# Performance work log

Measured on AMD Instinct MI355X. Metric: run time of the kernel, lower is better.

Reference implementation:

```python
import jax, jax.numpy as jnp
import numpy as np

N = 100_000      # nodes
E = 1_600_000    # edges
D_IN = 128       # input_dim
H = 128          # hidden_dim
L = 3            # num_layers
G = 128          # graphs in batch
EPS = 1e-5       # BatchNorm1d eps


def setup_inputs() -> dict:
    key = jax.random.key(0)
    ks = jax.random.split(key, 8)
    inp = {
        "x": jax.random.normal(ks[0], (N, D_IN), dtype=jnp.float32),
        "edge_index": jax.random.randint(ks[1], (2, E), 0, N),
        "batch": jnp.sort(jax.random.randint(ks[2], (N,), 0, G)),
    }
    for i in range(L):
        din = D_IN if i == 0 else H
        kw = jax.random.fold_in(key, 100 + i)
        inp[f"W{i}"] = jax.random.normal(kw, (din, H), dtype=jnp.float32) / np.sqrt(din).astype(np.float32)
        inp[f"b{i}"] = jnp.zeros((H,), jnp.float32)
        inp[f"g{i}"] = jnp.ones((H,), jnp.float32)
        inp[f"beta{i}"] = jnp.zeros((H,), jnp.float32)
    return inp


def _gcn_conv(x, W, b, src, dst, dinv):
    # GCNConv (normalize=True, add_self_loops=True):
    # out = D^{-1/2} (A + I) D^{-1/2} X W + b, deg computed on dst with self-loops
    h = x @ W                                   # [N,H]
    coef = (dinv[src] * dinv[dst])[:, None]     # per-edge norm
    agg = jax.ops.segment_sum(h[src] * coef, dst, num_segments=N)
    agg = agg + h * (dinv * dinv)[:, None]      # self-loop term deg^{-1}
    return agg + b


def _batchnorm(z, g, beta):
    mu = jnp.mean(z, axis=0)
    var = jnp.mean(jnp.square(z - mu), axis=0)  # biased var (training-mode BN)
    return (z - mu) * jax.lax.rsqrt(var + EPS) * g + beta


def reference(x, edge_index, batch,
              W0, b0, g0, beta0,
              W1, b1, g1, beta1,
              W2, b2, g2, beta2):
    src, dst = edge_index[0], edge_index[1]
    # degree of A + I on target index
    deg = jax.ops.segment_sum(jnp.ones((E,), x.dtype), dst, num_segments=N) + 1.0
    dinv = jax.lax.rsqrt(deg)
    params = [(W0, b0, g0, beta0), (W1, b1, g1, beta1), (W2, b2, g2, beta2)]
    zs = []
    h = x
    for (W, b, g, beta) in params:
        h = _gcn_conv(h, W, b, src, dst, dinv)
        h = jax.nn.relu(h)
        h = _batchnorm(h, g, beta)
        zs.append(h)
    pooled = [jax.ops.segment_sum(z, batch, num_segments=G) for z in zs]  # sum pool
    h_cat = jnp.concatenate(zs, axis=1)        # [N, L*H]
    g_cat = jnp.concatenate(pooled, axis=1)    # [G, L*H]
    return h_cat, g_cat
```

## Files before the change

kernel.cpp:

```cpp
#include <hip/hip_runtime.h>

#define NN 100000
#define NE 1600000
#define NG 128
#define BN_EPS 1e-5f
#define NBKT 64
#define AGG_BLOCKS 2048
#define AGG_WAVES (AGG_BLOCKS * 4)
#define NBUCK 98
#define BIN_BLOCKS 256
#define BIN_CHUNK 6250

typedef short s16x8 __attribute__((ext_vector_type(8)));
typedef float f32x4 __attribute__((ext_vector_type(4)));

static __device__ __forceinline__ unsigned short f2bf(float f) {
    unsigned u = __float_as_uint(f);
    u += 0x7fffu + ((u >> 16) & 1u);
    return (unsigned short)(u >> 16);
}
static __device__ __forceinline__ unsigned packbf(float a, float b) {
    return (unsigned)f2bf(a) | ((unsigned)f2bf(b) << 16);
}
static __device__ __forceinline__ float bf_lo(unsigned u) { return __uint_as_float(u << 16); }
static __device__ __forceinline__ float bf_hi(unsigned u) { return __uint_as_float(u & 0xffff0000u); }
static __device__ __forceinline__ float bf2f(ushort u) { return __uint_as_float((unsigned)u << 16); }

__global__ __launch_bounds__(256) void k_bhist(const int* __restrict__ dst, int* __restrict__ gbh) {
    __shared__ int lh[128];
    int t = threadIdx.x;
    if (t < 128) lh[t] = 0;
    __syncthreads();
    for (int e = blockIdx.x * 256 + t; e < NE; e += gridDim.x * 256)
        atomicAdd(&lh[dst[e] >> 10], 1);
    __syncthreads();
    if (t < 128 && lh[t]) atomicAdd(&gbh[t], lh[t]);
}

__global__ __launch_bounds__(128) void k_bscan(const int* __restrict__ gbh, int* __restrict__ gbase,
                                               int* __restrict__ gcur, int* __restrict__ row_start) {
    __shared__ int s[128];
    int t = threadIdx.x;
    int v = gbh[t];
    s[t] = v;
    __syncthreads();
    for (int o = 1; o < 128; o <<= 1) {
        int a = (t >= o) ? s[t - o] : 0;
        __syncthreads();
        s[t] += a;
        __syncthreads();
    }
    int ex = s[t] - v;
    gbase[t] = ex;
    gcur[t] = ex;
    if (t == 127) { gbase[128] = s[127]; row_start[NN] = NE; }
}

__global__ __launch_bounds__(256) void k_bin(const int* __restrict__ src, const int* __restrict__ dst,
                                             int* __restrict__ gcur, int* __restrict__ tmp) {
    __shared__ int lh[128], lb[128], lc[128];
    int t = threadIdx.x;
    if (t < 128) lh[t] = 0;
    __syncthreads();
    int e0 = blockIdx.x * BIN_CHUNK, e1 = e0 + BIN_CHUNK;
    for (int e = e0 + t; e < e1; e += 256) atomicAdd(&lh[dst[e] >> 10], 1);
    __syncthreads();
    if (t < 128) {
        int c = lh[t];
        lb[t] = c ? atomicAdd(&gcur[t], c) : 0;
        lc[t] = 0;
    }
    __syncthreads();
    for (int e = e0 + t; e < e1; e += 256) {
        int d = dst[e];
        int b = d >> 10;
        int off = atomicAdd(&lc[b], 1);
        tmp[lb[b] + off] = (src[e] << 10) | (d & 1023);
    }
}

__global__ __launch_bounds__(256) void k_csr(const int* __restrict__ tmp, const int* __restrict__ gbase,
                                             int* __restrict__ esrc, int* __restrict__ row_start,
                                             float* __restrict__ dinv) {
    __shared__ int h[1024], hs[1024], part[256];
    int b = blockIdx.x, t = threadIdx.x;
    int base = gbase[b], end = gbase[b + 1];
#pragma unroll
    for (int k = 0; k < 4; ++k) h[t * 4 + k] = 0;
    __syncthreads();
    for (int i = base + t; i < end; i += 256) atomicAdd(&h[tmp[i] & 1023], 1);
    __syncthreads();
    int l0 = h[t * 4], l1 = h[t * 4 + 1], l2 = h[t * 4 + 2], l3 = h[t * 4 + 3];
    int ssum = l0 + l1 + l2 + l3;
    part[t] = ssum;
    __syncthreads();
    for (int o = 1; o < 256; o <<= 1) {
        int a = (t >= o) ? part[t - o] : 0;
        __syncthreads();
        part[t] += a;
        __syncthreads();
    }
    int ex = part[t] - ssum;
    hs[t * 4]     = ex;
    hs[t * 4 + 1] = ex + l0;
    hs[t * 4 + 2] = ex + l0 + l1;
    hs[t * 4 + 3] = ex + l0 + l1 + l2;
    int n0 = b * 1024 + t * 4;
#pragma unroll
    for (int k = 0; k < 4; ++k) {
        int n = n0 + k;
        if (n < NN) {
            row_start[n] = base + hs[t * 4 + k];
            dinv[n] = rsqrtf((float)h[t * 4 + k] + 1.0f);
        }
    }
    __syncthreads();
    for (int i = base + t; i < end; i += 256) {
        int rec = tmp[i];
        int pos = atomicAdd(&hs[rec & 1023], 1);
        esrc[base + pos] = rec >> 10;
    }
}

__global__ __launch_bounds__(256) void k_cast(const float* __restrict__ x, uint4* __restrict__ xb) {
    int i = blockIdx.x * 256 + threadIdx.x;
    if (i >= NN * 16) return;
    float4 a = *(const float4*)(x + (size_t)i * 8);
    float4 b = *(const float4*)(x + (size_t)i * 8 + 4);
    uint4 o;
    o.x = packbf(a.x, a.y);
    o.y = packbf(a.z, a.w);
    o.z = packbf(b.x, b.y);
    o.w = packbf(b.z, b.w);
    xb[i] = o;
}

__global__ __launch_bounds__(64) void k_wfrag(const float* __restrict__ W, ushort* __restrict__ Wf) {
    int unit = blockIdx.x;
    int lane = threadIdx.x;
    int ks = unit >> 3, nb = unit & 7;
    int n = nb * 16 + (lane & 15);
    int k0 = ks * 32 + (lane >> 4) * 8;
    ushort o[8];
#pragma unroll
    for (int j = 0; j < 8; ++j) o[j] = f2bf(W[(size_t)(k0 + j) * 128 + n]);
    ushort* p = Wf + ((size_t)unit * 64 + lane) * 8;
#pragma unroll
    for (int j = 0; j < 8; ++j) p[j] = o[j];
}

__global__ __launch_bounds__(64) void k_wscale(const ushort* __restrict__ Wfb, const float* __restrict__ svec,
                                               ushort* __restrict__ Wff) {
    int unit = blockIdx.x;
    int lane = threadIdx.x;
    int k0 = (unit >> 3) * 32 + (lane >> 4) * 8;
    const ushort* p = Wfb + ((size_t)unit * 64 + lane) * 8;
    ushort* o = Wff + ((size_t)unit * 64 + lane) * 8;
#pragma unroll
    for (int j = 0; j < 8; ++j) o[j] = f2bf(bf2f(p[j]) * svec[k0 + j]);
}

__global__ __launch_bounds__(128) void k_finalize(const float* __restrict__ S, const float* __restrict__ Q,
                                                  const float* __restrict__ gam, const float* __restrict__ bet,
                                                  float* __restrict__ svec, float* __restrict__ tvec,
                                                  const float* __restrict__ Wnext, float* __restrict__ tW) {
    __shared__ float ts[128];
    int c = threadIdx.x;
    float s = 0.f, q = 0.f;
    for (int k = 0; k < NBKT; ++k) {
        s += S[k * 128 + c];
        q += Q[k * 128 + c];
    }
    float mean = s / (float)NN;
    float var = q / (float)NN - mean * mean;
    float rstd = rsqrtf(fmaxf(var, 0.f) + BN_EPS);
    float sc = gam[c] * rstd;
    float sh = bet[c] - mean * sc;
    svec[c] = sc;
    tvec[c] = sh;
    ts[c] = sh;
    __syncthreads();
    if (Wnext) {
        float acc = 0.f;
        for (int k = 0; k < 128; ++k) acc += ts[k] * Wnext[(size_t)k * 128 + c];
        tW[c] = acc;
    }
}

__global__ __launch_bounds__(256) void k_gemm(const ushort* __restrict__ Xb, const ushort* __restrict__ Wf,
                                              const float* __restrict__ tW, const float* __restrict__ dinv,
                                              ushort* __restrict__ hm) {
    int tid = threadIdx.x;
    int wid = tid >> 6, lane = tid & 63;
    int r0 = blockIdx.x * 64 + wid * 16;
    int m = lane & 15, g = lane >> 4;
    int xrow = r0 + m;
    int xr = (xrow < NN) ? xrow : (NN - 1);
    const ushort* Xrow = Xb + (size_t)xr * 128 + g * 8;
    f32x4 acc[8];
#pragma unroll
    for (int nb = 0; nb < 8; ++nb) acc[nb] = (f32x4){0.f, 0.f, 0.f, 0.f};
#pragma unroll
    for (int ks = 0; ks < 4; ++ks) {
        s16x8 af = *(const s16x8*)(Xrow + ks * 32);
#pragma unroll
        for (int nb = 0; nb < 8; ++nb) {
            s16x8 wf = *(const s16x8*)(Wf + ((size_t)(ks * 8 + nb) * 64 + lane) * 8);
            acc[nb] = __builtin_amdgcn_mfma_f32_16x16x32_bf16(wf, af, acc[nb], 0, 0, 0);
        }
    }
    if (xrow < NN) {
        float ds = dinv[xr];
        ushort* orow = hm + (size_t)xrow * 128 + g * 4;
        if (tW) {
#pragma unroll
            for (int nb = 0; nb < 8; ++nb) {
                float4 tw = *(const float4*)(tW + nb * 16 + g * 4);
                ushort4 o;
                o.x = f2bf(ds * (acc[nb][0] + tw.x));
                o.y = f2bf(ds * (acc[nb][1] + tw.y));
                o.z = f2bf(ds * (acc[nb][2] + tw.z));
                o.w = f2bf(ds * (acc[nb][3] + tw.w));
                *(ushort4*)(orow + nb * 16) = o;
            }
        } else {
#pragma unroll
            for (int nb = 0; nb < 8; ++nb) {
                ushort4 o;
                o.x = f2bf(ds * acc[nb][0]);
                o.y = f2bf(ds * acc[nb][1]);
                o.z = f2bf(ds * acc[nb][2]);
                o.w = f2bf(ds * acc[nb][3]);
                *(ushort4*)(orow + nb * 16) = o;
            }
        }
    }
}

__global__ __launch_bounds__(256) void k_agg(const uint* __restrict__ hm32, const int* __restrict__ esrc,
                                             const int* __restrict__ rs, const float* __restrict__ dinv,
                                             const float* __restrict__ bias, uint* __restrict__ act,
                                             float* __restrict__ bnsum, float* __restrict__ bnsq) {
    __shared__ float ls[128], lq[128];
    int tid = threadIdx.x;
    if (tid < 128) { ls[tid] = 0.f; lq[tid] = 0.f; }
    __syncthreads();
    int lane = tid & 63;
    int wgid = blockIdx.x * 4 + (tid >> 6);
    float2 b2 = *(const float2*)(bias + lane * 2);
    float s0 = 0.f, s1 = 0.f, q0 = 0.f, q1 = 0.f;

    for (int n = wgid; n < NN; n += AGG_WAVES) {
        uint self = hm32[(size_t)n * 64 + lane];
        float a0 = bf_lo(self);
        float a1 = bf_hi(self);

        int i  = __builtin_amdgcn_readfirstlane(rs[n]);
        int i1 = __builtin_amdgcn_readfirstlane(rs[n + 1]);

        int idxv = 0;
        if (i < i1) idxv = esrc[i + min(min(lane, 15), i1 - i - 1)];

        while (i < i1) {
            int cnt = i1 - i;
            cnt = (cnt > 16) ? 16 : cnt;
            int cur = idxv;
            int inext = i + cnt;
            if (inext < i1)
                idxv = esrc[inext + min(min(lane, 15), i1 - inext - 1)];
            uint g[16];
#pragma unroll
            for (int u = 0; u < 16; ++u) {
                int sidx = __builtin_amdgcn_readlane(cur, u);
                sidx = (u < cnt) ? sidx : NN;
                g[u] = hm32[(size_t)sidx * 64 + lane];
            }
#pragma unroll
            for (int u = 0; u < 16; ++u) {
                a0 += bf_lo(g[u]);
                a1 += bf_hi(g[u]);
            }
            i = inext;
        }
        float di = dinv[n];
        float z0 = fmaxf(fmaf(di, a0, b2.x), 0.f);
        float z1 = fmaxf(fmaf(di, a1, b2.y), 0.f);
        act[(size_t)n * 64 + lane] = packbf(z0, z1);
        s0 += z0; s1 += z1;
        q0 += z0 * z0; q1 += z1 * z1;
    }
    atomicAdd(&ls[lane * 2],     s0);
    atomicAdd(&ls[lane * 2 + 1], s1);
    atomicAdd(&lq[lane * 2],     q0);
    atomicAdd(&lq[lane * 2 + 1], q1);
    __syncthreads();
    if (tid < 128) {
        int bkt = blockIdx.x & (NBKT - 1);
        atomicAdd(&bnsum[bkt * 128 + tid], ls[tid]);
        atomicAdd(&bnsq[bkt * 128 + tid],  lq[tid]);
    }
}

__global__ __launch_bounds__(128) void k_norm(const ushort* __restrict__ act, const float* __restrict__ svec,
                                              const float* __restrict__ tvec, const int* __restrict__ batch,
                                              float* __restrict__ out, float* __restrict__ gout, int lofs) {
    int c = threadIdx.x;
    int n0 = blockIdx.x * 64;
    if (n0 >= NN) return;
    int n1 = n0 + 64; if (n1 > NN) n1 = NN;
    float scale = svec[c];
    float shift = tvec[c];
    int cur = batch[n0];
    float acc = 0.f;
    for (int n = n0; n < n1; ++n) {
        float z = bf2f(act[(size_t)n * 128 + c]) * scale + shift;
        out[(size_t)n * 384 + lofs + c] = z;
        int bn = batch[n];
        if (bn != cur) {
            atomicAdd(&gout[(size_t)cur * 384 + lofs + c], acc);
            acc = 0.f;
            cur = bn;
        }
        acc += z;
    }
    atomicAdd(&gout[(size_t)cur * 384 + lofs + c], acc);
}

extern "C" void kernel_launch(void* const* d_in, const int* in_sizes, int n_in,
                              void* d_out, int out_size, void* d_ws, size_t ws_size,
                              hipStream_t stream) {
    const float* x = (const float*)d_in[0];
    const int* ei = (const int*)d_in[1];
    const int* src = ei;
    const int* dst = ei + NE;
    const int* batch = (const int*)d_in[2];
    const float *W[3], *b[3], *g[3], *beta[3];
    for (int l = 0; l < 3; ++l) {
        W[l]    = (const float*)d_in[3 + 4 * l];
        b[l]    = (const float*)d_in[4 + 4 * l];
        g[l]    = (const float*)d_in[5 + 4 * l];
        beta[l] = (const float*)d_in[6 + 4 * l];
    }
    float* out = (float*)d_out;
    float* gout = out + (size_t)NN * 384;

    char* ws = (char*)d_ws;
    size_t off = 0;
    auto alloc = [&](size_t bytes) -> char* {
        off = (off + 255) & ~(size_t)255;
        char* p = ws + off;
        off += bytes;
        return p;
    };
    ushort* xb       = (ushort*)alloc((size_t)NN * 256);
    ushort* act      = (ushort*)alloc((size_t)NN * 256);
    ushort* hm       = (ushort*)alloc((size_t)(NN + 1) * 256);
    int*    esrc     = (int*)alloc((size_t)NE * 4);
    int*    tmp      = (int*)alloc((size_t)NE * 4);
    int*    row_start= (int*)alloc((size_t)(NN + 1) * 4);
    float*  dinv     = (float*)alloc((size_t)NN * 4);
    float*  bnst     = (float*)alloc((size_t)3 * 2 * NBKT * 128 * 4);
    ushort* Wf       = (ushort*)alloc(3 * 16384 * 2);
    ushort* Wff      = (ushort*)alloc(16384 * 2);
    float*  svt      = (float*)alloc(3 * 2 * 128 * 4);
    float*  tW       = (float*)alloc(128 * 4);
    int*    misc     = (int*)alloc(512 * 4);
    int* gbh   = misc;
    int* gbase = misc + 128;
    int* gcur  = misc + 384;
    (void)ws_size;

    hipMemsetAsync(gbh, 0, 128 * 4, stream);
    hipMemsetAsync(hm + (size_t)NN * 128, 0, 256, stream);
    hipMemsetAsync(bnst, 0, (size_t)3 * 2 * NBKT * 128 * 4, stream);
    hipMemsetAsync(gout, 0, (size_t)NG * 384 * 4, stream);

    k_bhist<<<512, 256, 0, stream>>>(dst, gbh);
    k_bscan<<<1, 128, 0, stream>>>(gbh, gbase, gcur, row_start);
    k_bin<<<BIN_BLOCKS, 256, 0, stream>>>(src, dst, gcur, tmp);
    k_csr<<<NBUCK, 256, 0, stream>>>(tmp, gbase, esrc, row_start, dinv);
    k_cast<<<(NN * 16 + 255) / 256, 256, 0, stream>>>(x, (uint4*)xb);
    for (int l = 0; l < 3; ++l) k_wfrag<<<32, 64, 0, stream>>>(W[l], Wf + l * 16384);

    for (int l = 0; l < 3; ++l) {
        float* S = bnst + (size_t)l * 2 * NBKT * 128;
        float* Q = S + NBKT * 128;
        float* sv = svt + l * 256;
        float* tv = sv + 128;
        const ushort* gin = (l == 0) ? xb : act;
        const ushort* wfrag = (l == 0) ? (Wf + 0) : Wff;
        const float* tw_in = (l == 0) ? nullptr : tW;

        k_gemm<<<(NN + 63) / 64, 256, 0, stream>>>(gin, wfrag, tw_in, dinv, hm);
        k_agg<<<AGG_BLOCKS, 256, 0, stream>>>((const uint*)hm, esrc, row_start, dinv, b[l],
                                              (uint*)act, S, Q);
        k_finalize<<<1, 128, 0, stream>>>(S, Q, g[l], beta[l], sv, tv,
                                          (l < 2) ? W[l + 1] : nullptr, tW);
        if (l < 2) k_wscale<<<32, 64, 0, stream>>>(Wf + (l + 1) * 16384, sv, Wff);
        k_norm<<<(NN + 63) / 64, 128, 0, stream>>>(act, sv, tv, batch, out, gout, l * 128);
    }
}
```

Before: 473.1 us.

## Fuse BN output into next-layer GEMM, per-graph pooling, merge finalize and wscale

The normalized output for layers 0 and 1 is now written inside the next layer's GEMM, reusing the bf16 activation tiles it already loads, and only the last layer keeps a standalone normalize kernel. Graph pooling becomes a per-graph reduction over sorted batch ranges (found by binary search) and is written directly instead of using atomics, which also removes the gout memset. BN finalize and weight rescaling are merged into one multi-block launch. The aggregation kernel processes two nodes per wave to raise memory-level parallelism, at the cost of more registers under a launch bound of 8.

```diff
diff --git a/kernel.cpp b/kernel.cpp
--- a/kernel.cpp
+++ b/kernel.cpp
@@ -149,47 +149,76 @@
     for (int j = 0; j < 8; ++j) p[j] = o[j];
 }
 
-__global__ __launch_bounds__(64) void k_wscale(const ushort* __restrict__ Wfb, const float* __restrict__ svec,
-                                               ushort* __restrict__ Wff) {
-    int unit = blockIdx.x;
-    int lane = threadIdx.x;
-    int k0 = (unit >> 3) * 32 + (lane >> 4) * 8;
-    const ushort* p = Wfb + ((size_t)unit * 64 + lane) * 8;
-    ushort* o = Wff + ((size_t)unit * 64 + lane) * 8;
-#pragma unroll
-    for (int j = 0; j < 8; ++j) o[j] = f2bf(bf2f(p[j]) * svec[k0 + j]);
-}
-
-__global__ __launch_bounds__(128) void k_finalize(const float* __restrict__ S, const float* __restrict__ Q,
-                                                  const float* __restrict__ gam, const float* __restrict__ bet,
-                                                  float* __restrict__ svec, float* __restrict__ tvec,
-                                                  const float* __restrict__ Wnext, float* __restrict__ tW) {
-    __shared__ float ts[128];
-    int c = threadIdx.x;
-    float s = 0.f, q = 0.f;
-    for (int k = 0; k < NBKT; ++k) {
-        s += S[k * 128 + c];
-        q += Q[k * 128 + c];
-    }
-    float mean = s / (float)NN;
-    float var = q / (float)NN - mean * mean;
-    float rstd = rsqrtf(fmaxf(var, 0.f) + BN_EPS);
-    float sc = gam[c] * rstd;
-    float sh = bet[c] - mean * sc;
-    svec[c] = sc;
-    tvec[c] = sh;
-    ts[c] = sh;
-    __syncthreads();
-    if (Wnext) {
-        float acc = 0.f;
-        for (int k = 0; k < 128; ++k) acc += ts[k] * Wnext[(size_t)k * 128 + c];
-        tW[c] = acc;
+__global__ __launch_bounds__(128) void k_gbounds(const int* __restrict__ batch, int* __restrict__ gb) {
+    int g = threadIdx.x;
+    int lo = 0, hi = NN;
+    while (lo < hi) {
+        int mid = (lo + hi) >> 1;
+        if (batch[mid] < g) lo = mid + 1; else hi = mid;
+    }
+    gb[g] = lo;
+    if (g == 0) gb[128] = NN;
+}
+
+__global__ __launch_bounds__(128) void k_finwscale(const float* __restrict__ S, const float* __restrict__ Q,
+                                                   const float* __restrict__ gam, const float* __restrict__ bet,
+                                                   float* __restrict__ svec, float* __restrict__ tvec,
+                                                   const float* __restrict__ Wnext, float* __restrict__ tW,
+                                                   const ushort* __restrict__ Wfb, ushort* __restrict__ Wff) {
+    int bid = blockIdx.x;
+    int t = threadIdx.x;
+    if (bid == 0) {
+        __shared__ float ts[128];
+        float s = 0.f, q = 0.f;
+        for (int k = 0; k < NBKT; ++k) {
+            s += S[k * 128 + t];
+            q += Q[k * 128 + t];
+        }
+        float mean = s / (float)NN;
+        float var = q / (float)NN - mean * mean;
+        float rstd = rsqrtf(fmaxf(var, 0.f) + BN_EPS);
+        float sc = gam[t] * rstd;
+        float sh = bet[t] - mean * sc;
+        svec[t] = sc;
+        tvec[t] = sh;
+        ts[t] = sh;
+        __syncthreads();
+        if (Wnext) {
+            float acc = 0.f;
+            for (int k = 0; k < 128; ++k) acc += ts[k] * Wnext[(size_t)k * 128 + t];
+            tW[t] = acc;
+        }
+    } else {
+        __shared__ float sv[32];
+        int unit = bid - 1;
+        int kbase = (unit >> 3) * 32;
+        if (t < 32) {
+            int c = kbase + t;
+            float s = 0.f, q = 0.f;
+            for (int k = 0; k < NBKT; ++k) {
+                s += S[k * 128 + c];
+                q += Q[k * 128 + c];
+            }
+            float mean = s / (float)NN;
+            float var = q / (float)NN - mean * mean;
+            sv[t] = gam[c] * rsqrtf(fmaxf(var, 0.f) + BN_EPS);
+        }
+        __syncthreads();
+        if (t < 64) {
+            int ko = (t >> 4) * 8;
+            const ushort* p = Wfb + ((size_t)unit * 64 + t) * 8;
+            ushort* o = Wff + ((size_t)unit * 64 + t) * 8;
+#pragma unroll
+            for (int j = 0; j < 8; ++j) o[j] = f2bf(bf2f(p[j]) * sv[ko + j]);
+        }
     }
 }
 
 __global__ __launch_bounds__(256) void k_gemm(const ushort* __restrict__ Xb, const ushort* __restrict__ Wf,
                                               const float* __restrict__ tW, const float* __restrict__ dinv,
-                                              ushort* __restrict__ hm) {
+                                              ushort* __restrict__ hm, const float* __restrict__ svec,
+                                              const float* __restrict__ tvec, float* __restrict__ outp,
+                                              int lofs) {
     int tid = threadIdx.x;
     int wid = tid >> 6, lane = tid & 63;
     int r0 = blockIdx.x * 64 + wid * 16;
@@ -197,16 +226,18 @@
     int xrow = r0 + m;
     int xr = (xrow < NN) ? xrow : (NN - 1);
     const ushort* Xrow = Xb + (size_t)xr * 128 + g * 8;
+    s16x8 af[4];
+#pragma unroll
+    for (int ks = 0; ks < 4; ++ks) af[ks] = *(const s16x8*)(Xrow + ks * 32);
     f32x4 acc[8];
 #pragma unroll
     for (int nb = 0; nb < 8; ++nb) acc[nb] = (f32x4){0.f, 0.f, 0.f, 0.f};
 #pragma unroll
     for (int ks = 0; ks < 4; ++ks) {
-        s16x8 af = *(const s16x8*)(Xrow + ks * 32);
 #pragma unroll
         for (int nb = 0; nb < 8; ++nb) {
             s16x8 wf = *(const s16x8*)(Wf + ((size_t)(ks * 8 + nb) * 64 + lane) * 8);
-            acc[nb] = __builtin_amdgcn_mfma_f32_16x16x32_bf16(wf, af, acc[nb], 0, 0, 0);
+            acc[nb] = __builtin_amdgcn_mfma_f32_16x16x32_bf16(wf, af[ks], acc[nb], 0, 0, 0);
         }
     }
     if (xrow < NN) {
@@ -234,13 +265,35 @@
                 *(ushort4*)(orow + nb * 16) = o;
             }
         }
-    }
-}
-
-__global__ __launch_bounds__(256) void k_agg(const uint* __restrict__ hm32, const int* __restrict__ esrc,
-                                             const int* __restrict__ rs, const float* __restrict__ dinv,
-                                             const float* __restrict__ bias, uint* __restrict__ act,
-                                             float* __restrict__ bnsum, float* __restrict__ bnsq) {
+        if (svec) {
+            float* zrow = outp + (size_t)xrow * 384 + lofs;
+#pragma unroll
+            for (int ks = 0; ks < 4; ++ks) {
+                int c0 = ks * 32 + g * 8;
+                float4 s0 = *(const float4*)(svec + c0);
+                float4 s1 = *(const float4*)(svec + c0 + 4);
+                float4 t0 = *(const float4*)(tvec + c0);
+                float4 t1 = *(const float4*)(tvec + c0 + 4);
+                float4 z0, z1;
+                z0.x = bf2f((ushort)af[ks][0]) * s0.x + t0.x;
+                z0.y = bf2f((ushort)af[ks][1]) * s0.y + t0.y;
+                z0.z = bf2f((ushort)af[ks][2]) * s0.z + t0.z;
+                z0.w = bf2f((ushort)af[ks][3]) * s0.w + t0.w;
+                z1.x = bf2f((ushort)af[ks][4]) * s1.x + t1.x;
+                z1.y = bf2f((ushort)af[ks][5]) * s1.y + t1.y;
+                z1.z = bf2f((ushort)af[ks][6]) * s1.z + t1.z;
+                z1.w = bf2f((ushort)af[ks][7]) * s1.w + t1.w;
+                *(float4*)(zrow + c0) = z0;
+                *(float4*)(zrow + c0 + 4) = z1;
+            }
+        }
+    }
+}
+
+__global__ __launch_bounds__(256, 8) void k_agg(const uint* __restrict__ hm32, const int* __restrict__ esrc,
+                                                const int* __restrict__ rs, const float* __restrict__ dinv,
+                                                const float* __restrict__ bias, uint* __restrict__ act,
+                                                float* __restrict__ bnsum, float* __restrict__ bnsq) {
     __shared__ float ls[128], lq[128];
     int tid = threadIdx.x;
     if (tid < 128) { ls[tid] = 0.f; lq[tid] = 0.f; }
@@ -250,44 +303,65 @@
     float2 b2 = *(const float2*)(bias + lane * 2);
     float s0 = 0.f, s1 = 0.f, q0 = 0.f, q1 = 0.f;
 
-    for (int n = wgid; n < NN; n += AGG_WAVES) {
-        uint self = hm32[(size_t)n * 64 + lane];
-        float a0 = bf_lo(self);
-        float a1 = bf_hi(self);
-
-        int i  = __builtin_amdgcn_readfirstlane(rs[n]);
-        int i1 = __builtin_amdgcn_readfirstlane(rs[n + 1]);
-
-        int idxv = 0;
-        if (i < i1) idxv = esrc[i + min(min(lane, 15), i1 - i - 1)];
-
-        while (i < i1) {
-            int cnt = i1 - i;
-            cnt = (cnt > 16) ? 16 : cnt;
-            int cur = idxv;
-            int inext = i + cnt;
-            if (inext < i1)
-                idxv = esrc[inext + min(min(lane, 15), i1 - inext - 1)];
-            uint g[16];
-#pragma unroll
-            for (int u = 0; u < 16; ++u) {
-                int sidx = __builtin_amdgcn_readlane(cur, u);
-                sidx = (u < cnt) ? sidx : NN;
-                g[u] = hm32[(size_t)sidx * 64 + lane];
-            }
-#pragma unroll
-            for (int u = 0; u < 16; ++u) {
-                a0 += bf_lo(g[u]);
-                a1 += bf_hi(g[u]);
-            }
-            i = inext;
-        }
-        float di = dinv[n];
-        float z0 = fmaxf(fmaf(di, a0, b2.x), 0.f);
-        float z1 = fmaxf(fmaf(di, a1, b2.y), 0.f);
-        act[(size_t)n * 64 + lane] = packbf(z0, z1);
-        s0 += z0; s1 += z1;
-        q0 += z0 * z0; q1 += z1 * z1;
+    for (int base = wgid * 2; base < NN; base += AGG_WAVES * 2) {
+        int nA = base, nB = base + 1;
+        uint selfA = hm32[(size_t)nA * 64 + lane];
+        uint selfB = hm32[(size_t)nB * 64 + lane];
+        float aA0 = bf_lo(selfA), aA1 = bf_hi(selfA);
+        float aB0 = bf_lo(selfB), aB1 = bf_hi(selfB);
+
+        int iA  = __builtin_amdgcn_readfirstlane(rs[nA]);
+        int iM  = __builtin_amdgcn_readfirstlane(rs[nA + 1]);
+        int iE  = __builtin_amdgcn_readfirstlane(rs[nB + 1]);
+        int iA1 = iM, iB = iM, iB1 = iE;
+
+        int idxA = 0, idxB = 0;
+        if (iA < iA1) idxA = esrc[iA + min(min(lane, 15), iA1 - iA - 1)];
+        if (iB < iB1) idxB = esrc[iB + min(min(lane, 15), iB1 - iB - 1)];
+
+        while (iA < iA1 || iB < iB1) {
+            int cntA = iA1 - iA; cntA = cntA > 16 ? 16 : (cntA < 0 ? 0 : cntA);
+            int cntB = iB1 - iB; cntB = cntB > 16 ? 16 : (cntB < 0 ? 0 : cntB);
+            int curA = idxA, curB = idxB;
+            int inA = iA + cntA, inB = iB + cntB;
+            if (inA < iA1) idxA = esrc[inA + min(min(lane, 15), iA1 - inA - 1)];
+            if (inB < iB1) idxB = esrc[inB + min(min(lane, 15), iB1 - inB - 1)];
+            uint gA[16], gB[16];
+            if (cntA) {
+#pragma unroll
+                for (int u = 0; u < 16; ++u) {
+                    int sx = __builtin_amdgcn_readlane(curA, u);
+                    sx = (u < cntA) ? sx : NN;
+                    gA[u] = hm32[(size_t)sx * 64 + lane];
+                }
+            }
+            if (cntB) {
+#pragma unroll
+                for (int u = 0; u < 16; ++u) {
+                    int sx = __builtin_amdgcn_readlane(curB, u);
+                    sx = (u < cntB) ? sx : NN;
+                    gB[u] = hm32[(size_t)sx * 64 + lane];
+                }
+            }
+            if (cntA) {
+#pragma unroll
+                for (int u = 0; u < 16; ++u) { aA0 += bf_lo(gA[u]); aA1 += bf_hi(gA[u]); }
+            }
+            if (cntB) {
+#pragma unroll
+                for (int u = 0; u < 16; ++u) { aB0 += bf_lo(gB[u]); aB1 += bf_hi(gB[u]); }
+            }
+            iA = inA; iB = inB;
+        }
+        float dA = dinv[nA], dB = dinv[nB];
+        float zA0 = fmaxf(fmaf(dA, aA0, b2.x), 0.f);
+        float zA1 = fmaxf(fmaf(dA, aA1, b2.y), 0.f);
+        float zB0 = fmaxf(fmaf(dB, aB0, b2.x), 0.f);
+        float zB1 = fmaxf(fmaf(dB, aB1, b2.y), 0.f);
+        act[(size_t)nA * 64 + lane] = packbf(zA0, zA1);
+        act[(size_t)nB * 64 + lane] = packbf(zB0, zB1);
+        s0 += zA0 + zB0; s1 += zA1 + zB1;
+        q0 += zA0 * zA0 + zB0 * zB0; q1 += zA1 * zA1 + zB1 * zB1;
     }
     atomicAdd(&ls[lane * 2],     s0);
     atomicAdd(&ls[lane * 2 + 1], s1);
@@ -301,29 +375,35 @@
     }
 }
 
-__global__ __launch_bounds__(128) void k_norm(const ushort* __restrict__ act, const float* __restrict__ svec,
-                                              const float* __restrict__ tvec, const int* __restrict__ batch,
-                                              float* __restrict__ out, float* __restrict__ gout, int lofs) {
+__global__ __launch_bounds__(256) void k_pool(const ushort* __restrict__ act, const float* __restrict__ svec,
+                                              const float* __restrict__ tvec, const int* __restrict__ gb,
+                                              float* __restrict__ gout, int lofs) {
+    __shared__ float ps[256];
+    int g = blockIdx.x;
+    int t = threadIdx.x;
+    int c = t & 127, half = t >> 7;
+    int gs = gb[g], ge = gb[g + 1];
+    float sum = 0.f;
+    for (int n = gs + half; n < ge; n += 2) sum += bf2f(act[(size_t)n * 128 + c]);
+    ps[t] = sum;
+    __syncthreads();
+    if (t < 128) {
+        float tot = ps[t] + ps[t + 128];
+        float cnt = (float)(ge - gs);
+        gout[(size_t)g * 384 + lofs + t] = svec[t] * tot + tvec[t] * cnt;
+    }
+}
+
+__global__ __launch_bounds__(128) void k_norm2(const ushort* __restrict__ act, const float* __restrict__ svec,
+                                               const float* __restrict__ tvec, float* __restrict__ outp) {
     int c = threadIdx.x;
     int n0 = blockIdx.x * 64;
     if (n0 >= NN) return;
     int n1 = n0 + 64; if (n1 > NN) n1 = NN;
     float scale = svec[c];
     float shift = tvec[c];
-    int cur = batch[n0];
-    float acc = 0.f;
-    for (int n = n0; n < n1; ++n) {
-        float z = bf2f(act[(size_t)n * 128 + c]) * scale + shift;
-        out[(size_t)n * 384 + lofs + c] = z;
-        int bn = batch[n];
-        if (bn != cur) {
-            atomicAdd(&gout[(size_t)cur * 384 + lofs + c], acc);
-            acc = 0.f;
-            cur = bn;
-        }
-        acc += z;
-    }
-    atomicAdd(&gout[(size_t)cur * 384 + lofs + c], acc);
+    for (int n = n0; n < n1; ++n)
+        outp[(size_t)n * 384 + 256 + c] = bf2f(act[(size_t)n * 128 + c]) * scale + shift;
 }
 
 extern "C" void kernel_launch(void* const* d_in, const int* in_sizes, int n_in,
@@ -364,16 +444,16 @@
     ushort* Wff      = (ushort*)alloc(16384 * 2);
     float*  svt      = (float*)alloc(3 * 2 * 128 * 4);
     float*  tW       = (float*)alloc(128 * 4);
-    int*    misc     = (int*)alloc(512 * 4);
+    int*    misc     = (int*)alloc(1024 * 4);
     int* gbh   = misc;
     int* gbase = misc + 128;
     int* gcur  = misc + 384;
+    int* gb    = misc + 512;
     (void)ws_size;
 
     hipMemsetAsync(gbh, 0, 128 * 4, stream);
     hipMemsetAsync(hm + (size_t)NN * 128, 0, 256, stream);
     hipMemsetAsync(bnst, 0, (size_t)3 * 2 * NBKT * 128 * 4, stream);
-    hipMemsetAsync(gout, 0, (size_t)NG * 384 * 4, stream);
 
     k_bhist<<<512, 256, 0, stream>>>(dst, gbh);
     k_bscan<<<1, 128, 0, stream>>>(gbh, gbase, gcur, row_start);
@@ -381,6 +461,7 @@
     k_csr<<<NBUCK, 256, 0, stream>>>(tmp, gbase, esrc, row_start, dinv);
     k_cast<<<(NN * 16 + 255) / 256, 256, 0, stream>>>(x, (uint4*)xb);
     for (int l = 0; l < 3; ++l) k_wfrag<<<32, 64, 0, stream>>>(W[l], Wf + l * 16384);
+    k_gbounds<<<1, 128, 0, stream>>>(batch, gb);
 
     for (int l = 0; l < 3; ++l) {
         float* S = bnst + (size_t)l * 2 * NBKT * 128;
@@ -390,13 +471,17 @@
         const ushort* gin = (l == 0) ? xb : act;
         const ushort* wfrag = (l == 0) ? (Wf + 0) : Wff;
         const float* tw_in = (l == 0) ? nullptr : tW;
-
-        k_gemm<<<(NN + 63) / 64, 256, 0, stream>>>(gin, wfrag, tw_in, dinv, hm);
+        const float* psv = (l == 0) ? nullptr : (svt + (l - 1) * 256);
+        const float* ptv = (l == 0) ? nullptr : (svt + (l - 1) * 256 + 128);
+
+        k_gemm<<<(NN + 63) / 64, 256, 0, stream>>>(gin, wfrag, tw_in, dinv, hm,
+                                                   psv, ptv, out, (l - 1) * 128);
         k_agg<<<AGG_BLOCKS, 256, 0, stream>>>((const uint*)hm, esrc, row_start, dinv, b[l],
                                               (uint*)act, S, Q);
-        k_finalize<<<1, 128, 0, stream>>>(S, Q, g[l], beta[l], sv, tv,
-                                          (l < 2) ? W[l + 1] : nullptr, tW);
-        if (l < 2) k_wscale<<<32, 64, 0, stream>>>(Wf + (l + 1) * 16384, sv, Wff);
-        k_norm<<<(NN + 63) / 64, 128, 0, stream>>>(act, sv, tv, batch, out, gout, l * 128);
-    }
-}
+        k_finwscale<<<(l < 2) ? 33 : 1, 128, 0, stream>>>(S, Q, g[l], beta[l], sv, tv,
+                                                          (l < 2) ? W[l + 1] : nullptr, tW,
+                                                          (l < 2) ? (Wf + (l + 1) * 16384) : nullptr, Wff);
+        k_pool<<<NG, 256, 0, stream>>>(act, sv, tv, gb, gout, l * 128);
+    }
+    k_norm2<<<(NN + 63) / 64, 128, 0, stream>>>(act, svt + 2 * 256, svt + 2 * 256 + 128, out);
+}
```

After: 853.8 us. 80.5% more time.
